# Optimization experiments

Measured on AMD Instinct MI355X. Metric: run time of the kernel, lower is better.

The kernel has to match this reference:

```python
import jax, jax.numpy as jnp
import numpy as np

K = 51           # kernel_size
DENSE_INNER = 2
EPS_LN = 1e-6
EPS_GRN = 1e-6

def _make_peripheral_coords(radius, dense_inner=2):
    coords = list(range(0, min(radius, dense_inner) + 1))
    v = 1
    while v < radius:
        v *= 2
        if v > dense_inner and v < radius:
            coords.append(v)
    if radius not in coords:
        coords.append(radius)
    return sorted(set(coords))

def _quantise(a, coords):
    q = 0
    for c in coords:
        if c <= a:
            q = c
        else:
            break
    return q

def _build_idx_map(kernel_size, dense_inner):
    radius = kernel_size // 2
    coords = _make_peripheral_coords(radius, dense_inner)
    signed = [-c for c in reversed(coords[1:])] + list(coords)
    P = len(signed)
    c2i = {c: i for i, c in enumerate(signed)}
    idx = []
    for i in range(kernel_size):
        oi = i - radius
        qi = _quantise(abs(oi), coords)
        ii = c2i[-qi if oi < 0 else qi]
        for j in range(kernel_size):
            oj = j - radius
            qj = _quantise(abs(oj), coords)
            jj = c2i[-qj if oj < 0 else qj]
            idx.append(ii * P + jj)
    return np.asarray(idx, dtype=np.int32), P

IDX_MAP, P = _build_idx_map(K, DENSE_INNER)  # P == 13 for K=51

DIM = 384
HID = 4 * DIM

def setup_inputs() -> dict:
    key = jax.random.key(0)
    ks = jax.random.split(key, 10)
    B, C, H, W = 8, DIM, 64, 64
    std = 0.02
    return {
        "x": jax.random.normal(ks[0], (B, C, H, W), jnp.float32),
        "weight_comp": jax.random.normal(ks[1], (C, P * P), jnp.float32) * std,
        "kpe": jax.random.normal(ks[2], (1, 1, K, K), jnp.float32) * std,
        "ln_w": jnp.ones((C,), jnp.float32),
        "ln_b": jnp.zeros((C,), jnp.float32),
        "w1": jax.random.normal(ks[3], (C, HID), jnp.float32) * std,
        "b1": jnp.zeros((HID,), jnp.float32),
        "grn_gamma": jax.random.normal(ks[4], (HID,), jnp.float32) * std,
        "grn_beta": jax.random.normal(ks[5], (HID,), jnp.float32) * std,
        "w2": jax.random.normal(ks[6], (HID, C), jnp.float32) * std,
        "b2": jnp.zeros((C,), jnp.float32),
    }

def _block(x, weight_comp, kpe, ln_w, ln_b, w1, b1, grn_gamma, grn_beta, w2, b2):
    C = x.shape[1]
    # gather-built peripheral depthwise kernel: (C, 1, K, K) + shared positional bias
    w = weight_comp[:, IDX_MAP].reshape(C, 1, K, K) + kpe
    y = jax.lax.conv_general_dilated(
        x, w, window_strides=(1, 1), padding=[(K // 2, K // 2)] * 2,
        feature_group_count=C, dimension_numbers=("NCHW", "OIHW", "NCHW"))
    h = y.transpose(0, 2, 3, 1)  # NHWC
    # LayerNorm (channels_last, biased variance, eps=1e-6)
    mu = jnp.mean(h, axis=-1, keepdims=True)
    var = jnp.mean(jnp.square(h - mu), axis=-1, keepdims=True)
    h = (h - mu) * jax.lax.rsqrt(var + EPS_LN) * ln_w + ln_b
    # pointwise MLP with GRN
    h = jnp.einsum("nhwc,cf->nhwf", h, w1) + b1
    h = jax.nn.gelu(h, approximate=False)  # nn.GELU default is exact erf form
    gx = jnp.sqrt(jnp.sum(jnp.square(h), axis=(1, 2), keepdims=True))  # (N,1,1,F)
    nx = gx / (jnp.mean(gx, axis=-1, keepdims=True) + EPS_GRN)
    h = grn_gamma * (h * nx) + grn_beta + h
    h = jnp.einsum("nhwf,fc->nhwc", h, w2) + b2
    return x + h.transpose(0, 3, 1, 2)

def reference(x, weight_comp, kpe, ln_w, ln_b, w1, b1, grn_gamma, grn_beta, w2, b2):
    return _block(x, weight_comp, kpe, ln_w, ln_b, w1, b1, grn_gamma, grn_beta, w2, b2)
```

## Files before the change

### kernel.cpp

```cpp
#include <hip/hip_runtime.h>

#define CDIM 384
#define FDIM 1536
#define KK 51
#define RAD 25
#define NPIX 32768
#define HW 4096

#define CSTR 136
#define OSTR 68

typedef float  f32x4  __attribute__((ext_vector_type(4)));
typedef short  short8 __attribute__((ext_vector_type(8)));
typedef __bf16 bf16x8 __attribute__((ext_vector_type(8)));
typedef unsigned short us4 __attribute__((ext_vector_type(4)));

__device__ __constant__ int AXIS[51] = {
  0,
  1,1,1,1,1,1,1,1,1,
  2,2,2,2,2,2,2,2,
  3,3,3,3,
  4,4,
  5,
  6,
  7,
  8,8,
  9,9,9,9,
  10,10,10,10,10,10,10,10,
  11,11,11,11,11,11,11,11,11,
  12
};

__device__ __forceinline__ unsigned short bf16_rn(float x){
  union { float f; unsigned u; } v; v.f = x;
  unsigned r = v.u + 0x7FFFu + ((v.u >> 16) & 1u);
  return (unsigned short)(r >> 16);
}
__device__ __forceinline__ unsigned short f2bf(float x){
  __bf16 h = (__bf16)x;
  return __builtin_bit_cast(unsigned short, h);
}
__device__ __forceinline__ float bf2f(unsigned short h){
  union { unsigned u; float f; } v; v.u = ((unsigned)h) << 16; return v.f;
}
__device__ __forceinline__ float gelu_f(float v){
  float t = v*(0.7978845608f + 0.0356774081f*v*v);
  float sg = 1.f/(1.f + __expf(-2.f*t));
  return v * sg;
}

__global__ __launch_bounds__(256) void k_prep(const float* __restrict__ wc,
                                              const float* __restrict__ kpe,
                                              float* __restrict__ wfull,
                                              const float* __restrict__ w1,
                                              unsigned short* __restrict__ w1T,
                                              const float* __restrict__ w2,
                                              unsigned short* __restrict__ w2T,
                                              const float* __restrict__ beta,
                                              const float* __restrict__ b2,
                                              float* __restrict__ c2,
                                              float* __restrict__ grn){
  __shared__ float tile[64][65];
  __shared__ float red[256];
  int bid = blockIdx.x;
  int tid = threadIdx.x;
  if (bid < 384){
    int c = bid;
    const float* wcc = wc + c*169;
    float* wo = wfull + (size_t)c*2601;
    for (int idx = tid; idx < 2601; idx += 256){
      int i = idx / 51, j = idx - i*51;
      wo[idx] = wcc[AXIS[i]*13 + AXIS[j]] + kpe[idx];
    }
  } else if (bid < 672){
    const float* src; unsigned short* dst; int R, C, t;
    if (bid < 528){ src = w1; dst = w1T; R = CDIM; C = FDIM; t = bid - 384; }
    else          { src = w2; dst = w2T; R = FDIM; C = CDIM; t = bid - 528; }
    int nct = C >> 6;
    int tc = t % nct, tr = t / nct;
    int r0 = tr*64, c0 = tc*64;
    int lane = tid & 63, q = tid >> 6;
    #pragma unroll
    for (int it = 0; it < 16; ++it){
      int r = it*4 + q;
      tile[r][lane] = src[(size_t)(r0 + r)*C + c0 + lane];
    }
    __syncthreads();
    #pragma unroll
    for (int it = 0; it < 16; ++it){
      int c = it*4 + q;
      dst[(size_t)(c0 + c)*R + r0 + lane] = f2bf(tile[lane][c]);
    }
  } else if (bid < 678){
    int lane = tid & 63, w = tid >> 6;
    int c = (bid - 672)*64 + lane;
    float s = 0.f;
    for (int f = w*384; f < (w + 1)*384; ++f)
      s += beta[f] * w2[(size_t)f*CDIM + c];
    red[w*64 + lane] = s;
    __syncthreads();
    if (tid < 64){
      float t = red[tid] + red[64 + tid] + red[128 + tid] + red[192 + tid];
      c2[c] = t + b2[c];
    }
  } else {
    for (int i = tid; i < 8*FDIM; i += 256) grn[i] = 0.f;
  }
}

__global__ __launch_bounds__(256) void k_conv_mfma(const float* __restrict__ x,
                                                   const float* __restrict__ wfull,
                                                   float* __restrict__ y){
  __shared__ __align__(16) float outb[64*OSTR];
  __shared__ __align__(16) unsigned short bufs[2][4][1088];
  int img = blockIdx.x;
  int ch  = img % CDIM;
  const float* xim = x + (size_t)img*HW;
  const float* wch = wfull + (size_t)ch*2601;
  int tid = threadIdx.x;
  int lane = tid & 63, wid = tid >> 6;
  int li = lane & 15, g = lane >> 4;
  int t0 = (lane & 31) << 2;
  int c0 = lane >> 5;

  for (int i = tid; i < 1088; i += 256)
    *(f32x4*)&outb[i*4] = (f32x4){0.f,0.f,0.f,0.f};

  bf16x8 Bf[4][2];
  #pragma unroll
  for (int nt = 0; nt < 4; ++nt){
    int i = nt*16 + li;
    #pragma unroll
    for (int kt = 0; kt < 2; ++kt){
      union { bf16x8 v; unsigned short u[8]; } tmp;
      #pragma unroll
      for (int e = 0; e < 8; ++e){
        int j = kt*32 + g*8 + e;
        float v = (i < 51 && j < 51) ? wch[i*51 + j] : 0.f;
        tmp.u[e] = bf16_rn(v);
      }
      Bf[nt][kt] = tmp.v;
    }
  }

  {
    const float* xr = xim + (16*wid)*64;
    #pragma unroll
    for (int it = 0; it < 4; ++it){
      int c = c0 + 2*it;
      us4 o;
      #pragma unroll
      for (int e = 0; e < 4; ++e){
        int xi = t0 + e + c - 25;
        float v = (xi >= 0 && xi < 64) ? xr[xi] : 0.f;
        o[e] = bf16_rn(v);
      }
      *(us4*)&bufs[0][wid][c*CSTR + t0] = o;
    }
  }
  __syncthreads();

  #pragma unroll 1
  for (int ph = 0; ph < 16; ++ph){
    float pf[16];
    if (ph + 1 < 16){
      const float* xr = xim + (ph + 1 + 16*wid)*64;
      #pragma unroll
      for (int it = 0; it < 4; ++it){
        int c = c0 + 2*it;
        #pragma unroll
        for (int e = 0; e < 4; ++e){
          int xi = t0 + e + c - 25;
          int xc = min(max(xi, 0), 63);
          pf[it*4 + e] = xr[xc];
        }
      }
    }

    bf16x8 Af[4][2];
    #pragma unroll
    for (int s = 0; s < 4; ++s){
      const unsigned short* bb = &bufs[ph & 1][s][0];
      #pragma unroll
      for (int kt = 0; kt < 2; ++kt){
        int u0 = wid*16 + kt*32 + g*8 + li;
        int c  = li & 7;
        Af[s][kt] = *(const bf16x8*)&bb[c*CSTR + (u0 - c)];
      }
    }

    #pragma unroll
    for (int dd = 0; dd < 6; ++dd){
      int d = dd - 2;
      int pmax = ph + 25 + 16*d;
      if (pmax < 0 || pmax > 78) continue;
      f32x4 V = {0.f,0.f,0.f,0.f};
      #pragma unroll
      for (int s = 0; s < 4; ++s){
        int nt = s - d;
        if (nt < 0 || nt > 3) continue;
        V = __builtin_amdgcn_mfma_f32_16x16x32_bf16(Af[s][0], Bf[nt][0], V, 0, 0, 0);
        V = __builtin_amdgcn_mfma_f32_16x16x32_bf16(Af[s][1], Bf[nt][1], V, 0, 0, 0);
      }
      int p = pmax - li;
      if (p >= 0 && p < 64){
        float* oa = &outb[p*OSTR + wid*16 + g*4];
        f32x4 old = *(const f32x4*)oa;
        *(f32x4*)oa = old + V;
      }
    }

    if (ph + 1 < 16){
      unsigned short* dst = &bufs[(ph + 1) & 1][wid][0];
      #pragma unroll
      for (int it = 0; it < 4; ++it){
        int c = c0 + 2*it;
        us4 o;
        #pragma unroll
        for (int e = 0; e < 4; ++e){
          int xi = t0 + e + c - 25;
          float v = (xi >= 0 && xi < 64) ? pf[it*4 + e] : 0.f;
          o[e] = bf16_rn(v);
        }
        *(us4*)&dst[c*CSTR + t0] = o;
      }
    }
    __syncthreads();
  }

  float* yo = y + (size_t)img*HW;
  #pragma unroll
  for (int k = 0; k < 4; ++k){
    int pix = k*1024 + tid*4;
    int p = pix >> 6, q = pix & 63;
    *(f32x4*)(yo + pix) = *(const f32x4*)&outb[p*OSTR + q];
  }
}

__global__ __launch_bounds__(256) void k_ln(const float* __restrict__ y,
                                            const float* __restrict__ lnw,
                                            const float* __restrict__ lnb,
                                            unsigned short* __restrict__ yn){
  __shared__ float sred[2][4][64];
  __shared__ unsigned short tile[384*66];
  int tid = threadIdx.x, lane = tid & 63, w = tid >> 6;
  int pg0 = blockIdx.x * 64;
  int b = pg0 >> 12, sp0 = pg0 & 4095;
  const float* yb = y + (size_t)b*CDIM*HW + sp0 + lane;
  int cbase = w * 96;
  float sum = 0.f, sq = 0.f;
  for (int cc = 0; cc < 96; ++cc){
    float v = yb[(size_t)(cbase + cc)*HW];
    sum += v; sq += v*v;
  }
  sred[0][w][lane] = sum; sred[1][w][lane] = sq;
  __syncthreads();
  float ts = 0.f, tq = 0.f;
  #pragma unroll
  for (int u = 0; u < 4; ++u){ ts += sred[0][u][lane]; tq += sred[1][u][lane]; }
  float mu   = ts * (1.f/CDIM);
  float var  = tq * (1.f/CDIM) - mu*mu;
  float rstd = rsqrtf(var + 1e-6f);
  for (int cc = 0; cc < 96; ++cc){
    int c = cbase + cc;
    float v = (yb[(size_t)c*HW] - mu) * rstd * lnw[c] + lnb[c];
    tile[c*66 + lane] = f2bf(v);
  }
  __syncthreads();
  for (int pp = 0; pp < 16; ++pp){
    int p = w*16 + pp;
    size_t orow = (size_t)(pg0 + p)*CDIM;
    #pragma unroll
    for (int chk = 0; chk < 6; ++chk){
      yn[orow + chk*64 + lane] = tile[(chk*64 + lane)*66 + p];
    }
  }
}

__global__ __launch_bounds__(256) void k_gemm1p(const unsigned short* __restrict__ A,
                                                const unsigned short* __restrict__ BT,
                                                const float* __restrict__ b1,
                                                unsigned short* __restrict__ H,
                                                float* __restrict__ grn){
  __shared__ __align__(16) unsigned short pan[64*392];
  __shared__ __align__(16) unsigned short bS[2][128*40];
  int m0 = blockIdx.x * 64;
  int img = m0 >> 12;
  int tid = threadIdx.x;
  int lane = tid & 63, wid = tid >> 6;
  int wr = wid >> 1, wc = wid & 1;
  int lm = lane & 15, g = lane >> 4;
  int sr = tid & 127, sc = tid >> 7;

  #pragma unroll
  for (int t = 0; t < 12; ++t){
    int idx = tid + 256*t;
    int row = idx / 48, ch = idx - row*48;
    *(short8*)&pan[row*392 + ch*8] = *(const short8*)(A + (size_t)(m0 + row)*CDIM + ch*8);
  }

  {
    const unsigned short* gb = BT + (size_t)sr*CDIM + sc*16;
    *(short8*)&bS[0][sr*40 + sc*16]     = *(const short8*)(gb);
    *(short8*)&bS[0][sr*40 + sc*16 + 8] = *(const short8*)(gb + 8);
  }
  short8 rn0, rn1;
  {
    const unsigned short* gb = BT + (size_t)sr*CDIM + 32 + sc*16;
    rn0 = *(const short8*)(gb);
    rn1 = *(const short8*)(gb + 8);
  }
  int pft = 0, pk = 64;
  int par = 0;

  #pragma unroll 1
  for (int ft = 0; ft < 12; ++ft){
    f32x4 acc[2][4];
    #pragma unroll
    for (int i = 0; i < 2; ++i)
      #pragma unroll
      for (int j = 0; j < 4; ++j) acc[i][j] = (f32x4){0.f,0.f,0.f,0.f};

    #pragma unroll 1
    for (int ks = 0; ks < 12; ++ks){
      int k0 = ks*32;
      __syncthreads();
      if (!(ft == 11 && ks == 11)){
        *(short8*)&bS[par^1][sr*40 + sc*16]     = rn0;
        *(short8*)&bS[par^1][sr*40 + sc*16 + 8] = rn1;
      }
      if (!(ft == 11 && ks >= 10)){
        const unsigned short* gb = BT + (size_t)(pft*128 + sr)*CDIM + pk + sc*16;
        rn0 = *(const short8*)(gb);
        rn1 = *(const short8*)(gb + 8);
        pk += 32; if (pk == CDIM){ pk = 0; ++pft; }
      }
      bf16x8 aF[2], bF[4];
      #pragma unroll
      for (int fm = 0; fm < 2; ++fm) aF[fm] = *(const bf16x8*)&pan[(wr*32 + fm*16 + lm)*392 + k0 + g*8];
      #pragma unroll
      for (int fn = 0; fn < 4; ++fn) bF[fn] = *(const bf16x8*)&bS[par][(wc*64 + fn*16 + lm)*40 + g*8];
      #pragma unroll
      for (int fm = 0; fm < 2; ++fm)
        #pragma unroll
        for (int fn = 0; fn < 4; ++fn)
          acc[fm][fn] = __builtin_amdgcn_mfma_f32_16x16x32_bf16(aF[fm], bF[fn], acc[fm][fn], 0, 0, 0);
      par ^= 1;
    }

    int n0 = ft*128;
    float psum[4] = {0.f,0.f,0.f,0.f};
    #pragma unroll
    for (int fn = 0; fn < 4; ++fn){
      int n = n0 + wc*64 + fn*16 + lm;
      float bias = b1[n];
      #pragma unroll
      for (int fm = 0; fm < 2; ++fm){
        int mb = m0 + wr*32 + fm*16 + g*4;
        #pragma unroll
        for (int r = 0; r < 4; ++r){
          float v = gelu_f(acc[fm][fn][r] + bias);
          H[(size_t)(mb + r)*FDIM + n] = f2bf(v);
          psum[fn] += v*v;
        }
      }
    }
    #pragma unroll
    for (int fn = 0; fn < 4; ++fn){
      float v = psum[fn];
      v += __shfl_xor(v, 16);
      v += __shfl_xor(v, 32);
      if (g == 0){
        atomicAdd(&grn[img*FDIM + n0 + wc*64 + fn*16 + lm], v);
      }
    }
  }
}

__global__ __launch_bounds__(256) void k_grn(const float* __restrict__ grn,
                                             const float* __restrict__ gamma,
                                             float* __restrict__ S){
  int n = blockIdx.x;
  const float* g = grn + n*FDIM;
  __shared__ float red[256];
  float p = 0.f;
  for (int f = threadIdx.x; f < FDIM; f += 256) p += sqrtf(g[f]);
  red[threadIdx.x] = p;
  __syncthreads();
  for (int s = 128; s > 0; s >>= 1){
    if (threadIdx.x < s) red[threadIdx.x] += red[threadIdx.x + s];
    __syncthreads();
  }
  float mean = red[0] * (1.f/FDIM);
  float inv = 1.f/(mean + 1e-6f);
  for (int f = threadIdx.x; f < FDIM; f += 256){
    float nx = sqrtf(g[f]) * inv;
    S[n*FDIM + f] = 1.f + gamma[f]*nx;
  }
}

__global__ __launch_bounds__(256) void k_gemm2(const unsigned short* __restrict__ W2T,
                                               const unsigned short* __restrict__ H,
                                               const float* __restrict__ S,
                                               const float* __restrict__ c2,
                                               const float* __restrict__ xg,
                                               float* __restrict__ out){
  __shared__ __align__(16) unsigned short aS[2][128*40];
  __shared__ __align__(16) unsigned short bS[2][128*40];
  int bid = blockIdx.x;
  int x8 = bid & 7;
  int kk = bid >> 3;
  int bm = kk % 3;
  int bn = x8 + 8*(kk / 3);
  int c0 = bm*128, p0 = bn*128;
  int img = p0 >> 12;
  const float* Simg = S + img*FDIM;
  int tid = threadIdx.x;
  int lane = tid & 63, wid = tid >> 6;
  int wr = wid >> 1, wc = wid & 1;
  int lm = lane & 15, g = lane >> 4;
  int sr = tid & 127, sc = tid >> 7;
  f32x4 acc[4][4];
  #pragma unroll
  for (int i = 0; i < 4; ++i)
    #pragma unroll
    for (int j = 0; j < 4; ++j) acc[i][j] = (f32x4){0.f,0.f,0.f,0.f};

  {
    const unsigned short* ga = W2T + (size_t)(c0 + sr)*FDIM + sc*16;
    *(short8*)&aS[0][sr*40 + sc*16]     = *(const short8*)(ga);
    *(short8*)&aS[0][sr*40 + sc*16 + 8] = *(const short8*)(ga + 8);
    const unsigned short* gb = H + (size_t)(p0 + sr)*FDIM + sc*16;
    short8 h0 = *(const short8*)(gb);
    short8 h1 = *(const short8*)(gb + 8);
    const float* sv = Simg + sc*16;
    short8 o0, o1;
    #pragma unroll
    for (int e = 0; e < 8; ++e){
      o0[e] = (short)f2bf(bf2f((unsigned short)h0[e]) * sv[e]);
      o1[e] = (short)f2bf(bf2f((unsigned short)h1[e]) * sv[e+8]);
    }
    *(short8*)&bS[0][sr*40 + sc*16]     = o0;
    *(short8*)&bS[0][sr*40 + sc*16 + 8] = o1;
  }
  short8 ra0, ra1, rh0, rh1;
  f32x4 rs0, rs1, rs2, rs3;
  {
    const unsigned short* ga = W2T + (size_t)(c0 + sr)*FDIM + 32 + sc*16;
    ra0 = *(const short8*)(ga); ra1 = *(const short8*)(ga + 8);
    const unsigned short* gb = H + (size_t)(p0 + sr)*FDIM + 32 + sc*16;
    rh0 = *(const short8*)(gb); rh1 = *(const short8*)(gb + 8);
    const float* sv = Simg + 32 + sc*16;
    rs0 = *(const f32x4*)(sv);      rs1 = *(const f32x4*)(sv + 4);
    rs2 = *(const f32x4*)(sv + 8);  rs3 = *(const f32x4*)(sv + 12);
  }
  int par = 0;

  #pragma unroll 1
  for (int ks = 0; ks < 48; ++ks){
    __syncthreads();
    if (ks + 1 < 48){
      *(short8*)&aS[par^1][sr*40 + sc*16]     = ra0;
      *(short8*)&aS[par^1][sr*40 + sc*16 + 8] = ra1;
      short8 o0, o1;
      float se[16];
      #pragma unroll
      for (int e = 0; e < 4; ++e){ se[e]=rs0[e]; se[4+e]=rs1[e]; se[8+e]=rs2[e]; se[12+e]=rs3[e]; }
      #pragma unroll
      for (int e = 0; e < 8; ++e){
        o0[e] = (short)f2bf(bf2f((unsigned short)rh0[e]) * se[e]);
        o1[e] = (short)f2bf(bf2f((unsigned short)rh1[e]) * se[e+8]);
      }
      *(short8*)&bS[par^1][sr*40 + sc*16]     = o0;
      *(short8*)&bS[par^1][sr*40 + sc*16 + 8] = o1;
    }
    if (ks + 2 < 48){
      int nk = (ks + 2)*32;
      const unsigned short* ga = W2T + (size_t)(c0 + sr)*FDIM + nk + sc*16;
      ra0 = *(const short8*)(ga); ra1 = *(const short8*)(ga + 8);
      const unsigned short* gb = H + (size_t)(p0 + sr)*FDIM + nk + sc*16;
      rh0 = *(const short8*)(gb); rh1 = *(const short8*)(gb + 8);
      const float* sv = Simg + nk + sc*16;
      rs0 = *(const f32x4*)(sv);      rs1 = *(const f32x4*)(sv + 4);
      rs2 = *(const f32x4*)(sv + 8);  rs3 = *(const f32x4*)(sv + 12);
    }
    bf16x8 aF[4], bF[4];
    #pragma unroll
    for (int fm = 0; fm < 4; ++fm) aF[fm] = *(const bf16x8*)&aS[par][(wr*64 + fm*16 + lm)*40 + g*8];
    #pragma unroll
    for (int fn = 0; fn < 4; ++fn) bF[fn] = *(const bf16x8*)&bS[par][(wc*64 + fn*16 + lm)*40 + g*8];
    #pragma unroll
    for (int fm = 0; fm < 4; ++fm)
      #pragma unroll
      for (int fn = 0; fn < 4; ++fn)
        acc[fm][fn] = __builtin_amdgcn_mfma_f32_16x16x32_bf16(aF[fm], bF[fn], acc[fm][fn], 0, 0, 0);
    par ^= 1;
  }

  int sp0 = p0 & 4095;
  #pragma unroll
  for (int fn = 0; fn < 4; ++fn){
    int pixoff = sp0 + wc*64 + fn*16 + lm;
    #pragma unroll
    for (int fm = 0; fm < 4; ++fm){
      #pragma unroll
      for (int r = 0; r < 4; ++r){
        int c = c0 + wr*64 + fm*16 + g*4 + r;
        size_t addr = ((size_t)img*CDIM + c)*HW + pixoff;
        out[addr] = acc[fm][fn][r] + c2[c] + xg[addr];
      }
    }
  }
}

extern "C" void kernel_launch(void* const* d_in, const int* in_sizes, int n_in,
                              void* d_out, int out_size, void* d_ws, size_t ws_size,
                              hipStream_t stream) {
  const float* x    = (const float*)d_in[0];
  const float* wc   = (const float*)d_in[1];
  const float* kpe  = (const float*)d_in[2];
  const float* lnw  = (const float*)d_in[3];
  const float* lnb  = (const float*)d_in[4];
  const float* w1   = (const float*)d_in[5];
  const float* b1   = (const float*)d_in[6];
  const float* gam  = (const float*)d_in[7];
  const float* beta = (const float*)d_in[8];
  const float* w2   = (const float*)d_in[9];
  const float* b2   = (const float*)d_in[10];
  float* out = (float*)d_out;

  char* ws = (char*)d_ws;
  size_t o = 0;
  auto take = [&](size_t bytes)->char*{
    char* p = ws + o;
    o = (o + bytes + 511) & ~(size_t)511;
    return p;
  };
  float*          y     = out;
  float*          wfull = (float*)take((size_t)CDIM*2601*4);
  unsigned short* yn    = (unsigned short*)take((size_t)NPIX*CDIM*2);
  unsigned short* H     = (unsigned short*)take((size_t)NPIX*FDIM*2);
  unsigned short* w1T   = (unsigned short*)take((size_t)CDIM*FDIM*2);
  unsigned short* w2T   = (unsigned short*)take((size_t)CDIM*FDIM*2);
  float*          grn   = (float*)take(8*FDIM*4);
  float*          S     = (float*)take(8*FDIM*4);
  float*          c2    = (float*)take(CDIM*4);
  if (o > ws_size) return;

  k_prep<<<679, 256, 0, stream>>>(wc, kpe, wfull, w1, w1T, w2, w2T, beta, b2, c2, grn);
  k_conv_mfma<<<3072, 256, 0, stream>>>(x, wfull, y);
  k_ln<<<NPIX/64, 256, 0, stream>>>(y, lnw, lnb, yn);
  k_gemm1p<<<NPIX/64, 256, 0, stream>>>(yn, w1T, b1, H, grn);
  k_grn<<<8, 256, 0, stream>>>(grn, gam, S);
  k_gemm2<<<3*(NPIX/128), 256, 0, stream>>>(w2T, H, S, c2, x, out);
}
```

Before: 402.0 us.

## Fuse LayerNorm into GEMM1 prologue and fold GRN scale into per-image W2

The standalone LayerNorm kernel is removed. GEMM1 now reads the fp32 conv output directly, computes per-pixel mean and variance, and writes normalized bf16 rows straight into its shared-memory panel, which avoids the yn round trip through global memory. The per-feature GRN scale is no longer applied to H inside GEMM2's inner loop. A new small kernel instead pre-multiplies W2 by the per-image scale, producing eight scaled weight copies, so GEMM2 becomes a plain bf16 GEMM. The risks are higher register pressure from holding 96 floats per thread in GEMM1, an extra 9 MB scaled-weight buffer, and slightly different bf16 rounding.

```diff
diff --git a/kernel.cpp b/kernel.cpp
--- a/kernel.cpp
+++ b/kernel.cpp
@@ -237,53 +237,16 @@
   }
 }
 
-__global__ __launch_bounds__(256) void k_ln(const float* __restrict__ y,
-                                            const float* __restrict__ lnw,
-                                            const float* __restrict__ lnb,
-                                            unsigned short* __restrict__ yn){
-  __shared__ float sred[2][4][64];
-  __shared__ unsigned short tile[384*66];
-  int tid = threadIdx.x, lane = tid & 63, w = tid >> 6;
-  int pg0 = blockIdx.x * 64;
-  int b = pg0 >> 12, sp0 = pg0 & 4095;
-  const float* yb = y + (size_t)b*CDIM*HW + sp0 + lane;
-  int cbase = w * 96;
-  float sum = 0.f, sq = 0.f;
-  for (int cc = 0; cc < 96; ++cc){
-    float v = yb[(size_t)(cbase + cc)*HW];
-    sum += v; sq += v*v;
-  }
-  sred[0][w][lane] = sum; sred[1][w][lane] = sq;
-  __syncthreads();
-  float ts = 0.f, tq = 0.f;
-  #pragma unroll
-  for (int u = 0; u < 4; ++u){ ts += sred[0][u][lane]; tq += sred[1][u][lane]; }
-  float mu   = ts * (1.f/CDIM);
-  float var  = tq * (1.f/CDIM) - mu*mu;
-  float rstd = rsqrtf(var + 1e-6f);
-  for (int cc = 0; cc < 96; ++cc){
-    int c = cbase + cc;
-    float v = (yb[(size_t)c*HW] - mu) * rstd * lnw[c] + lnb[c];
-    tile[c*66 + lane] = f2bf(v);
-  }
-  __syncthreads();
-  for (int pp = 0; pp < 16; ++pp){
-    int p = w*16 + pp;
-    size_t orow = (size_t)(pg0 + p)*CDIM;
-    #pragma unroll
-    for (int chk = 0; chk < 6; ++chk){
-      yn[orow + chk*64 + lane] = tile[(chk*64 + lane)*66 + p];
-    }
-  }
-}
-
-__global__ __launch_bounds__(256) void k_gemm1p(const unsigned short* __restrict__ A,
+__global__ __launch_bounds__(256) void k_gemm1p(const float* __restrict__ y,
+                                                const float* __restrict__ lnw,
+                                                const float* __restrict__ lnb,
                                                 const unsigned short* __restrict__ BT,
                                                 const float* __restrict__ b1,
                                                 unsigned short* __restrict__ H,
                                                 float* __restrict__ grn){
   __shared__ __align__(16) unsigned short pan[64*392];
   __shared__ __align__(16) unsigned short bS[2][128*40];
+  __shared__ float sred[2][4][64];
   int m0 = blockIdx.x * 64;
   int img = m0 >> 12;
   int tid = threadIdx.x;
@@ -292,11 +255,35 @@
   int lm = lane & 15, g = lane >> 4;
   int sr = tid & 127, sc = tid >> 7;
 
-  #pragma unroll
-  for (int t = 0; t < 12; ++t){
-    int idx = tid + 256*t;
-    int row = idx / 48, ch = idx - row*48;
-    *(short8*)&pan[row*392 + ch*8] = *(const short8*)(A + (size_t)(m0 + row)*CDIM + ch*8);
+  {
+    int sp0 = m0 & 4095;
+    const float* yb = y + (size_t)img*CDIM*HW + sp0 + lane;
+    int cbase = wid*96;
+    float v[96];
+    float sum = 0.f, sq = 0.f;
+    #pragma unroll
+    for (int cc = 0; cc < 96; ++cc){
+      float t = yb[(size_t)(cbase + cc)*HW];
+      v[cc] = t; sum += t; sq += t*t;
+    }
+    sred[0][wid][lane] = sum; sred[1][wid][lane] = sq;
+    __syncthreads();
+    float ts = 0.f, tq = 0.f;
+    #pragma unroll
+    for (int u = 0; u < 4; ++u){ ts += sred[0][u][lane]; tq += sred[1][u][lane]; }
+    float mu   = ts * (1.f/CDIM);
+    float rstd = rsqrtf(tq * (1.f/CDIM) - mu*mu + 1e-6f);
+    #pragma unroll
+    for (int j = 0; j < 12; ++j){
+      short8 o;
+      #pragma unroll
+      for (int e = 0; e < 8; ++e){
+        int c = cbase + j*8 + e;
+        float t = (v[j*8 + e] - mu) * rstd * lnw[c] + lnb[c];
+        o[e] = (short)f2bf(t);
+      }
+      *(short8*)&pan[lane*392 + cbase + j*8] = o;
+    }
   }
 
   {
@@ -399,9 +386,23 @@
   }
 }
 
-__global__ __launch_bounds__(256) void k_gemm2(const unsigned short* __restrict__ W2T,
+__global__ __launch_bounds__(256) void k_scale(const unsigned short* __restrict__ w2T,
+                                               const float* __restrict__ S,
+                                               unsigned short* __restrict__ W2s){
+  int img = blockIdx.y;
+  size_t base = ((size_t)blockIdx.x*256 + threadIdx.x)*8;
+  int f0 = (int)(base % FDIM);
+  const float* Si = S + img*FDIM + f0;
+  short8 wv = *(const short8*)(w2T + base);
+  short8 o;
+  #pragma unroll
+  for (int e = 0; e < 8; ++e)
+    o[e] = (short)f2bf(bf2f((unsigned short)wv[e]) * Si[e]);
+  *(short8*)(W2s + (size_t)img*CDIM*FDIM + base) = o;
+}
+
+__global__ __launch_bounds__(256) void k_gemm2(const unsigned short* __restrict__ W2s,
                                                const unsigned short* __restrict__ H,
-                                               const float* __restrict__ S,
                                                const float* __restrict__ c2,
                                                const float* __restrict__ xg,
                                                float* __restrict__ out){
@@ -414,7 +415,7 @@
   int bn = x8 + 8*(kk / 3);
   int c0 = bm*128, p0 = bn*128;
   int img = p0 >> 12;
-  const float* Simg = S + img*FDIM;
+  const unsigned short* Wimg = W2s + (size_t)img*CDIM*FDIM;
   int tid = threadIdx.x;
   int lane = tid & 63, wid = tid >> 6;
   int wr = wid >> 1, wc = wid & 1;
@@ -427,32 +428,19 @@
     for (int j = 0; j < 4; ++j) acc[i][j] = (f32x4){0.f,0.f,0.f,0.f};
 
   {
-    const unsigned short* ga = W2T + (size_t)(c0 + sr)*FDIM + sc*16;
+    const unsigned short* ga = Wimg + (size_t)(c0 + sr)*FDIM + sc*16;
     *(short8*)&aS[0][sr*40 + sc*16]     = *(const short8*)(ga);
     *(short8*)&aS[0][sr*40 + sc*16 + 8] = *(const short8*)(ga + 8);
     const unsigned short* gb = H + (size_t)(p0 + sr)*FDIM + sc*16;
-    short8 h0 = *(const short8*)(gb);
-    short8 h1 = *(const short8*)(gb + 8);
-    const float* sv = Simg + sc*16;
-    short8 o0, o1;
-    #pragma unroll
-    for (int e = 0; e < 8; ++e){
-      o0[e] = (short)f2bf(bf2f((unsigned short)h0[e]) * sv[e]);
-      o1[e] = (short)f2bf(bf2f((unsigned short)h1[e]) * sv[e+8]);
-    }
-    *(short8*)&bS[0][sr*40 + sc*16]     = o0;
-    *(short8*)&bS[0][sr*40 + sc*16 + 8] = o1;
+    *(short8*)&bS[0][sr*40 + sc*16]     = *(const short8*)(gb);
+    *(short8*)&bS[0][sr*40 + sc*16 + 8] = *(const short8*)(gb + 8);
   }
   short8 ra0, ra1, rh0, rh1;
-  f32x4 rs0, rs1, rs2, rs3;
   {
-    const unsigned short* ga = W2T + (size_t)(c0 + sr)*FDIM + 32 + sc*16;
+    const unsigned short* ga = Wimg + (size_t)(c0 + sr)*FDIM + 32 + sc*16;
     ra0 = *(const short8*)(ga); ra1 = *(const short8*)(ga + 8);
     const unsigned short* gb = H + (size_t)(p0 + sr)*FDIM + 32 + sc*16;
     rh0 = *(const short8*)(gb); rh1 = *(const short8*)(gb + 8);
-    const float* sv = Simg + 32 + sc*16;
-    rs0 = *(const f32x4*)(sv);      rs1 = *(const f32x4*)(sv + 4);
-    rs2 = *(const f32x4*)(sv + 8);  rs3 = *(const f32x4*)(sv + 12);
   }
   int par = 0;
 
@@ -462,27 +450,15 @@
     if (ks + 1 < 48){
       *(short8*)&aS[par^1][sr*40 + sc*16]     = ra0;
       *(short8*)&aS[par^1][sr*40 + sc*16 + 8] = ra1;
-      short8 o0, o1;
-      float se[16];
-      #pragma unroll
-      for (int e = 0; e < 4; ++e){ se[e]=rs0[e]; se[4+e]=rs1[e]; se[8+e]=rs2[e]; se[12+e]=rs3[e]; }
-      #pragma unroll
-      for (int e = 0; e < 8; ++e){
-        o0[e] = (short)f2bf(bf2f((unsigned short)rh0[e]) * se[e]);
-        o1[e] = (short)f2bf(bf2f((unsigned short)rh1[e]) * se[e+8]);
-      }
-      *(short8*)&bS[par^1][sr*40 + sc*16]     = o0;
-      *(short8*)&bS[par^1][sr*40 + sc*16 + 8] = o1;
+      *(short8*)&bS[par^1][sr*40 + sc*16]     = rh0;
+      *(short8*)&bS[par^1][sr*40 + sc*16 + 8] = rh1;
     }
     if (ks + 2 < 48){
       int nk = (ks + 2)*32;
-      const unsigned short* ga = W2T + (size_t)(c0 + sr)*FDIM + nk + sc*16;
+      const unsigned short* ga = Wimg + (size_t)(c0 + sr)*FDIM + nk + sc*16;
       ra0 = *(const short8*)(ga); ra1 = *(const short8*)(ga + 8);
       const unsigned short* gb = H + (size_t)(p0 + sr)*FDIM + nk + sc*16;
       rh0 = *(const short8*)(gb); rh1 = *(const short8*)(gb + 8);
-      const float* sv = Simg + nk + sc*16;
-      rs0 = *(const f32x4*)(sv);      rs1 = *(const f32x4*)(sv + 4);
-      rs2 = *(const f32x4*)(sv + 8);  rs3 = *(const f32x4*)(sv + 12);
     }
     bf16x8 aF[4], bF[4];
     #pragma unroll
@@ -538,10 +514,10 @@
   };
   float*          y     = out;
   float*          wfull = (float*)take((size_t)CDIM*2601*4);
-  unsigned short* yn    = (unsigned short*)take((size_t)NPIX*CDIM*2);
   unsigned short* H     = (unsigned short*)take((size_t)NPIX*FDIM*2);
   unsigned short* w1T   = (unsigned short*)take((size_t)CDIM*FDIM*2);
   unsigned short* w2T   = (unsigned short*)take((size_t)CDIM*FDIM*2);
+  unsigned short* W2s   = (unsigned short*)take((size_t)8*CDIM*FDIM*2);
   float*          grn   = (float*)take(8*FDIM*4);
   float*          S     = (float*)take(8*FDIM*4);
   float*          c2    = (float*)take(CDIM*4);
@@ -549,8 +525,8 @@
 
   k_prep<<<679, 256, 0, stream>>>(wc, kpe, wfull, w1, w1T, w2, w2T, beta, b2, c2, grn);
   k_conv_mfma<<<3072, 256, 0, stream>>>(x, wfull, y);
-  k_ln<<<NPIX/64, 256, 0, stream>>>(y, lnw, lnb, yn);
-  k_gemm1p<<<NPIX/64, 256, 0, stream>>>(yn, w1T, b1, H, grn);
+  k_gemm1p<<<NPIX/64, 256, 0, stream>>>(y, lnw, lnb, w1T, b1, H, grn);
   k_grn<<<8, 256, 0, stream>>>(grn, gam, S);
-  k_gemm2<<<3*(NPIX/128), 256, 0, stream>>>(w2T, H, S, c2, x, out);
-}
+  k_scale<<<dim3(288, 8), 256, 0, stream>>>(w2T, S, W2s);
+  k_gemm2<<<3*(NPIX/128), 256, 0, stream>>>(W2s, H, c2, x, out);
+}
```

Measured after the change: 373.2 us, median of 2. 1.08x faster.
